# Kernel tuning notes

Measured on AMD Instinct MI355X. Metric: run time of the kernel, lower is better.

## Reference

```python
import jax, jax.numpy as jnp
import numpy as np

N = 50000      # nodes
DEG = 32       # fixed out-degree used to build a synthetic CSR graph
E = N * DEG    # edges
F = 64         # in_feats = n_hidden = out_feats
K = 3          # n_kernels
DIM = 2        # pseudo-coordinate projection dim
L = 3          # n_layers + 1 GMMConv layers


def setup_inputs() -> dict:
    key = jax.random.key(0)
    ks = jax.random.split(key, 8)
    feat = jax.random.normal(ks[0], (N, F), jnp.float32)
    pseudo = jax.random.uniform(ks[1], (E, 2), jnp.float32)  # per-edge pseudo coords
    rowptr = jnp.arange(N + 1, dtype=jnp.int32) * DEG        # CSR row pointers
    colind = jax.random.randint(ks[2], (E,), 0, N, jnp.int32)  # neighbor (src) ids
    # Per-layer parameters, stacked over L layers (all layers are FxF here).
    proj_W = 0.5 * jax.random.normal(ks[3], (L, 2, DIM), jnp.float32)   # pseudo_proj Linear weight
    proj_b = jnp.zeros((L, DIM), jnp.float32)                            # pseudo_proj Linear bias
    fc_W = jax.random.normal(ks[4], (L, F, K * F), jnp.float32) / np.sqrt(F)  # GMMConv fc (no bias)
    mu = jax.random.normal(ks[5], (L, K, DIM), jnp.float32)              # Gaussian means
    inv_sigma = jnp.ones((L, K, DIM), jnp.float32)                       # inverse std-devs
    return {"feat": feat, "pseudo": pseudo, "rowptr": rowptr, "colind": colind,
            "proj_W": proj_W, "proj_b": proj_b, "fc_W": fc_W, "mu": mu,
            "inv_sigma": inv_sigma}


def reference(feat, pseudo, rowptr, colind, proj_W, proj_b, fc_W, mu, inv_sigma):
    n = feat.shape[0]
    e = colind.shape[0]
    n_layers = fc_W.shape[0]
    n_kern = mu.shape[1]
    # dst node of each edge from CSR rowptr (edge e belongs to row i iff rowptr[i] <= e < rowptr[i+1])
    dst = jnp.searchsorted(rowptr, jnp.arange(e, dtype=rowptr.dtype), side="right") - 1

    h = feat
    for i in range(n_layers):  # small fixed layer loop
        # pseudo_proj: Linear(2, dim) + Tanh, per edge -> [E, DIM]
        u = jnp.tanh(pseudo @ proj_W[i] + proj_b[i])
        # Gaussian kernel weights: w[e,k] = exp(-0.5 * sum_d ((u - mu)^2 * inv_sigma^2)) -> [E, K]
        diff = u[:, None, :] - mu[i][None, :, :]
        w = jnp.exp(-0.5 * jnp.sum(diff * diff * (inv_sigma[i][None, :, :] ** 2), axis=-1))
        out_dim = fc_W[i].shape[1] // n_kern
        hp = (h @ fc_W[i]).reshape(n, n_kern, out_dim)  # [N, K, out]
        # message per edge: sum_k w[e,k] * hp[src(e), k, :]; loop over small K to avoid [E,K,out]
        msg = jnp.zeros((e, out_dim), h.dtype)
        for k in range(n_kern):
            msg = msg + w[:, k:k + 1] * hp[colind, k, :]
        # scatter-reduce (sum aggregation) into destination nodes
        h = jax.ops.segment_sum(msg, dst, num_segments=n)
        # dropout is identity in eval mode (p=0.0)
    return h
```

## Files before the change

kernel.cpp:

```cpp
#include <hip/hip_runtime.h>
#include <math.h>

#define FEAT 64
#define NKERN 3

typedef __attribute__((ext_vector_type(8))) short short8;
typedef __attribute__((ext_vector_type(4))) float float4v;
typedef __attribute__((ext_vector_type(2))) float float2v;

__device__ __forceinline__ unsigned short f2bf(float f) {
    unsigned int u = __float_as_uint(f);
    u = (u + 0x7fffu + ((u >> 16) & 1u)) >> 16;
    return (unsigned short)u;
}
__device__ __forceinline__ float bf2f(unsigned short b) {
    return __uint_as_float(((unsigned int)b) << 16);
}
__device__ __forceinline__ float fast_tanh(float x) {
    float e = __expf(2.f * x);
    return fmaf(-2.f, __builtin_amdgcn_rcpf(e + 1.f), 1.f);
}
__device__ __forceinline__ float sxor16(float v) {
    return __shfl_xor(v, 16, 64);
}

__global__ __launch_bounds__(256) void prep_kernel(
    const float* __restrict__ x, unsigned short* __restrict__ y, int n4,
    const float* __restrict__ fcW,
    unsigned short* __restrict__ Bth, unsigned short* __restrict__ Btl,
    int totalW, int nCastBlocks)
{
    int b = blockIdx.x;
    if (b < nCastBlocks) {
        int i = b * 256 + threadIdx.x;
        if (i >= n4) return;
        float4 v = ((const float4*)x)[i];
        ushort4 o;
        o.x = f2bf(v.x); o.y = f2bf(v.y); o.z = f2bf(v.z); o.w = f2bf(v.w);
        ((ushort4*)y)[i] = o;
    } else {
        int idx = (b - nCastBlocks) * 256 + threadIdx.x;
        if (idx >= totalW) return;
        int l   = idx / (FEAT * 192);
        int rem = idx - l * (FEAT * 192);
        int f   = rem / 192;
        int jp  = rem - f * 192;
        int k = jp >> 6, j = jp & 63;
        float v = fcW[(size_t)l * 12288 + j * 192 + k * 64 + f];
        unsigned short hi = f2bf(v);
        int dst = l * 12288 +
                  ((((f >> 4) * 6 + (jp >> 5)) * 4 + ((jp >> 3) & 3)) * 16 + (f & 15)) * 8 +
                  (jp & 7);
        Bth[dst] = hi;
        Btl[dst] = f2bf(v - bf2f(hi));
    }
}

__global__ __launch_bounds__(512, 8) void layer_kernel(
    const unsigned short* __restrict__ h,
    const int*   __restrict__ rowptr,
    const int*   __restrict__ colind,
    const float* __restrict__ pseudo,
    const float* __restrict__ projW,
    const float* __restrict__ projB,
    const float* __restrict__ mu,
    const float* __restrict__ isg,
    int layer,
    const unsigned short* __restrict__ Bth,
    const unsigned short* __restrict__ Btl,
    float* __restrict__ out,
    unsigned short* __restrict__ hnext,
    int n_nodes, int last_layer)
{
    __shared__ __align__(16) unsigned short Atile[3264];
    __shared__ __align__(16) unsigned int   Wlds[8][2][132];
    int tid  = threadIdx.x;
    int wv   = tid >> 6;
    int lane = tid & 63;
    int t0   = blockIdx.x * 16;

    const float* pw = projW + layer * 4;
    const float* pb = projB + layer * 2;
    const float* mm = mu  + layer * 6;
    const float* ss = isg + layer * 6;
    float pw0 = pw[0], pw1 = pw[1], pw2 = pw[2], pw3 = pw[3];
    float pb0 = pb[0], pb1 = pb[1];
    float m0 = mm[0], m1 = mm[1], m2 = mm[2], m3 = mm[3], m4 = mm[4], m5 = mm[5];
    float c0 = -0.5f * ss[0] * ss[0], c1 = -0.5f * ss[1] * ss[1];
    float c2 = -0.5f * ss[2] * ss[2], c3 = -0.5f * ss[3] * ss[3];
    float c4 = -0.5f * ss[4] * ss[4], c5 = -0.5f * ss[5] * ss[5];

    int half = lane >> 5;
    int p    = lane & 31;
    const char* hb = (const char*)h;

    int node = t0 + wv * 2 + half;
    int ncl  = node < n_nodes - 1 ? node : (n_nodes - 1);
    int rp   = rowptr[ncl];
    int deg  = rowptr[ncl + 1] - rp;
    bool fast = __all((deg == 32) && (node < n_nodes));
    if (fast) {
        int ei = rp + p;
        int cc = colind[ei];
        float2 ps = ((const float2*)pseudo)[ei];
        float u0 = fast_tanh(fmaf(ps.x, pw0, fmaf(ps.y, pw2, pb0)));
        float u1 = fast_tanh(fmaf(ps.x, pw1, fmaf(ps.y, pw3, pb1)));
        float d0 = u0 - m0, d1 = u1 - m1;
        float w0v = __expf(fmaf(d0 * d0, c0, d1 * d1 * c1));
        d0 = u0 - m2; d1 = u1 - m3;
        float w1v = __expf(fmaf(d0 * d0, c2, d1 * d1 * c3));
        d0 = u0 - m4; d1 = u1 - m5;
        float w2v = __expf(fmaf(d0 * d0, c4, d1 * d1 * c5));
        uint4 recw;
        recw.x = ((unsigned int)cc) << 7;
        recw.y = __float_as_uint(w0v);
        recw.z = __float_as_uint(w1v);
        recw.w = __float_as_uint(w2v);
        *(uint4*)&Wlds[wv][half][p * 4] = recw;

        int sub = (lane >> 4) & 1;
        int ch  = lane & 15;
        unsigned int fo = (unsigned int)(ch * 8);
        const unsigned int* Wg = &Wlds[wv][half][0];

        float2v a0l = {0.f,0.f}, a0h = {0.f,0.f};
        float2v a1l = {0.f,0.f}, a1h = {0.f,0.f};
        float2v a2l = {0.f,0.f}, a2h = {0.f,0.f};

        #pragma unroll
        for (int i = 0; i < 16; ++i) {
            int e = sub * 16 + i;
            uint4 rc = *(const uint4*)(Wg + e * 4);
            uint2 hv = *(const uint2*)(hb + (rc.x + fo));
            float2v vlo, vhi;
            vlo.x = __uint_as_float(hv.x << 16);
            vlo.y = __uint_as_float(hv.x & 0xffff0000u);
            vhi.x = __uint_as_float(hv.y << 16);
            vhi.y = __uint_as_float(hv.y & 0xffff0000u);
            float w0 = __uint_as_float(rc.y);
            float w1 = __uint_as_float(rc.z);
            float w2 = __uint_as_float(rc.w);
            float2v s0 = {w0, w0}, s1 = {w1, w1}, s2 = {w2, w2};
            a0l = __builtin_elementwise_fma(vlo, s0, a0l);
            a0h = __builtin_elementwise_fma(vhi, s0, a0h);
            a1l = __builtin_elementwise_fma(vlo, s1, a1l);
            a1h = __builtin_elementwise_fma(vhi, s1, a1h);
            a2l = __builtin_elementwise_fma(vlo, s2, a2l);
            a2h = __builtin_elementwise_fma(vhi, s2, a2h);
        }

        a0l.x += sxor16(a0l.x); a0l.y += sxor16(a0l.y);
        a0h.x += sxor16(a0h.x); a0h.y += sxor16(a0h.y);
        a1l.x += sxor16(a1l.x); a1l.y += sxor16(a1l.y);
        a1h.x += sxor16(a1h.x); a1h.y += sxor16(a1h.y);
        a2l.x += sxor16(a2l.x); a2l.y += sxor16(a2l.y);
        a2h.x += sxor16(a2h.x); a2h.y += sxor16(a2h.y);

        if (sub == 0) {
            int m  = wv * 2 + half;
            int j0 = ch * 4;
            int sa = (j0 >> 5) * 544 + ((j0 >> 3) & 3) * 136 + m * 8 + (j0 & 7);
            unsigned int k0l, k0h, k1l, k1h, k2l, k2h;
            asm("v_cvt_pk_bf16_f32 %0, %1, %2" : "=v"(k0l) : "v"(a0l.x), "v"(a0l.y));
            asm("v_cvt_pk_bf16_f32 %0, %1, %2" : "=v"(k0h) : "v"(a0h.x), "v"(a0h.y));
            asm("v_cvt_pk_bf16_f32 %0, %1, %2" : "=v"(k1l) : "v"(a1l.x), "v"(a1l.y));
            asm("v_cvt_pk_bf16_f32 %0, %1, %2" : "=v"(k1h) : "v"(a1h.x), "v"(a1h.y));
            asm("v_cvt_pk_bf16_f32 %0, %1, %2" : "=v"(k2l) : "v"(a2l.x), "v"(a2l.y));
            asm("v_cvt_pk_bf16_f32 %0, %1, %2" : "=v"(k2h) : "v"(a2h.x), "v"(a2h.y));
            uint2 w0 = {k0l, k0h}, w1 = {k1l, k1h}, w2 = {k2l, k2h};
            *(uint2*)&Atile[sa]        = w0;
            *(uint2*)&Atile[sa + 1088] = w1;
            *(uint2*)&Atile[sa + 2176] = w2;
        }
    } else {
        for (int mq = 0; mq < 2; ++mq) {
            int node2 = t0 + wv * 2 + mq;
            float a0 = 0.f, a1 = 0.f, a2 = 0.f;
            if (node2 < n_nodes) {
                int nu = __builtin_amdgcn_readfirstlane(node2);
                int r0 = rowptr[nu];
                int dg = rowptr[nu + 1] - r0;
                for (int i = 0; i < dg; ++i) {
                    int cc = colind[r0 + i];
                    float px = pseudo[(size_t)(r0 + i) * 2];
                    float py = pseudo[(size_t)(r0 + i) * 2 + 1];
                    float u0 = fast_tanh(fmaf(px, pw0, fmaf(py, pw2, pb0)));
                    float u1 = fast_tanh(fmaf(px, pw1, fmaf(py, pw3, pb1)));
                    float d0 = u0 - m0, d1 = u1 - m1;
                    float w0e = __expf(fmaf(d0 * d0, c0, d1 * d1 * c1));
                    d0 = u0 - m2; d1 = u1 - m3;
                    float w1e = __expf(fmaf(d0 * d0, c2, d1 * d1 * c3));
                    d0 = u0 - m4; d1 = u1 - m5;
                    float w2e = __expf(fmaf(d0 * d0, c4, d1 * d1 * c5));
                    float vf = bf2f(h[(size_t)cc * FEAT + lane]);
                    a0 = fmaf(w0e, vf, a0);
                    a1 = fmaf(w1e, vf, a1);
                    a2 = fmaf(w2e, vf, a2);
                }
            }
            int sb = (lane >> 5) * 544 + ((lane >> 3) & 3) * 136 + (wv * 2 + mq) * 8 + (lane & 7);
            Atile[sb]        = f2bf(a0);
            Atile[sb + 1088] = f2bf(a1);
            Atile[sb + 2176] = f2bf(a2);
        }
    }
    __syncthreads();

    if (wv < 4) {
        int q  = lane >> 4;
        int nn = lane & 15;
        const unsigned short* bt0 = Bth + (((wv * 6) * 4 + q) * 16 + nn) * 8;
        const unsigned short* bt1 = Btl + (((wv * 6) * 4 + q) * 16 + nn) * 8;
        float4v acc = (float4v){0.f, 0.f, 0.f, 0.f};
        #pragma unroll
        for (int ks = 0; ks < 6; ++ks) {
            short8 ah = *(const short8*)&Atile[ks * 544 + q * 136 + nn * 8];
            short8 bh = *(const short8*)(bt0 + ks * 512);
            short8 bl = *(const short8*)(bt1 + ks * 512);
            acc = __builtin_amdgcn_mfma_f32_16x16x32_bf16(ah, bh, acc, 0, 0, 0);
            acc = __builtin_amdgcn_mfma_f32_16x16x32_bf16(ah, bl, acc, 0, 0, 0);
        }
        #pragma unroll
        for (int r = 0; r < 4; ++r) {
            int row = t0 + q * 4 + r;
            if (row < n_nodes) {
                if (last_layer)
                    out[(size_t)row * 64 + wv * 16 + nn] = acc[r];
                else
                    hnext[(size_t)row * 64 + wv * 16 + nn] = f2bf(acc[r]);
            }
        }
    }
}

extern "C" void kernel_launch(void* const* d_in, const int* in_sizes, int n_in,
                              void* d_out, int out_size, void* d_ws, size_t ws_size,
                              hipStream_t stream)
{
    const float* feat   = (const float*)d_in[0];
    const float* pseudo = (const float*)d_in[1];
    const int*   rowptr = (const int*)d_in[2];
    const int*   colind = (const int*)d_in[3];
    const float* projW  = (const float*)d_in[4];
    const float* projB  = (const float*)d_in[5];
    const float* fcW    = (const float*)d_in[6];
    const float* mu     = (const float*)d_in[7];
    const float* isg    = (const float*)d_in[8];
    float* out = (float*)d_out;

    int n  = in_sizes[0] / FEAT;
    int n_layers = in_sizes[6] / (FEAT * NKERN * FEAT);

    unsigned short* hbA = (unsigned short*)d_ws;
    unsigned short* hbB = hbA + (size_t)n * FEAT;
    unsigned short* Bth = hbB + (size_t)n * FEAT;
    unsigned short* Btl = Bth + (size_t)n_layers * 12288;

    int n4 = n * FEAT / 4;
    int totalW = n_layers * FEAT * 192;
    int castBlocks = (n4 + 255) / 256;
    int wpBlocks   = (totalW + 255) / 256;

    dim3 blk(256);
    dim3 prepGrid(castBlocks + wpBlocks);
    dim3 layerGrid((n + 15) / 16);
    dim3 layerBlk(512);

    prep_kernel<<<prepGrid, blk, 0, stream>>>(
        feat, hbA, n4, fcW, Bth, Btl, totalW, castBlocks);

    const unsigned short* hin = hbA;
    for (int l = 0; l < n_layers; ++l) {
        int last = (l == n_layers - 1);
        unsigned short* hb_out = (l == 0) ? hbB : hbA;
        layer_kernel<<<layerGrid, layerBlk, 0, stream>>>(
            hin, rowptr, colind, pseudo, projW, projB, mu, isg, l,
            Bth + (size_t)l * 12288, Btl + (size_t)l * 12288,
            out, hb_out, n, last);
        hin = hb_out;
    }
}
```

Before: 172.2 us.

## Split fused gather+MFMA layer kernel into separate gather and matmul kernels

```diff
diff --git a/kernel.cpp b/kernel.cpp
--- a/kernel.cpp
+++ b/kernel.cpp
@@ -56,7 +56,7 @@
     }
 }
 
-__global__ __launch_bounds__(512, 8) void layer_kernel(
+__global__ __launch_bounds__(512, 8) void gather_kernel(
     const unsigned short* __restrict__ h,
     const int*   __restrict__ rowptr,
     const int*   __restrict__ colind,
@@ -66,18 +66,15 @@
     const float* __restrict__ mu,
     const float* __restrict__ isg,
     int layer,
-    const unsigned short* __restrict__ Bth,
-    const unsigned short* __restrict__ Btl,
-    float* __restrict__ out,
-    unsigned short* __restrict__ hnext,
-    int n_nodes, int last_layer)
-{
-    __shared__ __align__(16) unsigned short Atile[3264];
-    __shared__ __align__(16) unsigned int   Wlds[8][2][132];
+    unsigned short* __restrict__ agg,
+    int n_nodes)
+{
+    __shared__ __align__(16) unsigned int Wlds[8][2][132];
     int tid  = threadIdx.x;
     int wv   = tid >> 6;
     int lane = tid & 63;
     int t0   = blockIdx.x * 16;
+    unsigned short* at = agg + (size_t)blockIdx.x * 3072;
 
     const float* pw = projW + layer * 4;
     const float* pb = projB + layer * 2;
@@ -159,7 +156,7 @@
         if (sub == 0) {
             int m  = wv * 2 + half;
             int j0 = ch * 4;
-            int sa = (j0 >> 5) * 544 + ((j0 >> 3) & 3) * 136 + m * 8 + (j0 & 7);
+            int sa = (j0 >> 5) * 512 + ((j0 >> 3) & 3) * 128 + m * 8 + (j0 & 7);
             unsigned int k0l, k0h, k1l, k1h, k2l, k2h;
             asm("v_cvt_pk_bf16_f32 %0, %1, %2" : "=v"(k0l) : "v"(a0l.x), "v"(a0l.y));
             asm("v_cvt_pk_bf16_f32 %0, %1, %2" : "=v"(k0h) : "v"(a0h.x), "v"(a0h.y));
@@ -168,9 +165,9 @@
             asm("v_cvt_pk_bf16_f32 %0, %1, %2" : "=v"(k2l) : "v"(a2l.x), "v"(a2l.y));
             asm("v_cvt_pk_bf16_f32 %0, %1, %2" : "=v"(k2h) : "v"(a2h.x), "v"(a2h.y));
             uint2 w0 = {k0l, k0h}, w1 = {k1l, k1h}, w2 = {k2l, k2h};
-            *(uint2*)&Atile[sa]        = w0;
-            *(uint2*)&Atile[sa + 1088] = w1;
-            *(uint2*)&Atile[sa + 2176] = w2;
+            *(uint2*)&at[sa]        = w0;
+            *(uint2*)&at[sa + 1024] = w1;
+            *(uint2*)&at[sa + 2048] = w2;
         }
     } else {
         for (int mq = 0; mq < 2; ++mq) {
@@ -198,37 +195,49 @@
                     a2 = fmaf(w2e, vf, a2);
                 }
             }
-            int sb = (lane >> 5) * 544 + ((lane >> 3) & 3) * 136 + (wv * 2 + mq) * 8 + (lane & 7);
-            Atile[sb]        = f2bf(a0);
-            Atile[sb + 1088] = f2bf(a1);
-            Atile[sb + 2176] = f2bf(a2);
-        }
-    }
-    __syncthreads();
-
-    if (wv < 4) {
-        int q  = lane >> 4;
-        int nn = lane & 15;
-        const unsigned short* bt0 = Bth + (((wv * 6) * 4 + q) * 16 + nn) * 8;
-        const unsigned short* bt1 = Btl + (((wv * 6) * 4 + q) * 16 + nn) * 8;
-        float4v acc = (float4v){0.f, 0.f, 0.f, 0.f};
-        #pragma unroll
-        for (int ks = 0; ks < 6; ++ks) {
-            short8 ah = *(const short8*)&Atile[ks * 544 + q * 136 + nn * 8];
-            short8 bh = *(const short8*)(bt0 + ks * 512);
-            short8 bl = *(const short8*)(bt1 + ks * 512);
-            acc = __builtin_amdgcn_mfma_f32_16x16x32_bf16(ah, bh, acc, 0, 0, 0);
-            acc = __builtin_amdgcn_mfma_f32_16x16x32_bf16(ah, bl, acc, 0, 0, 0);
-        }
-        #pragma unroll
-        for (int r = 0; r < 4; ++r) {
-            int row = t0 + q * 4 + r;
-            if (row < n_nodes) {
-                if (last_layer)
-                    out[(size_t)row * 64 + wv * 16 + nn] = acc[r];
-                else
-                    hnext[(size_t)row * 64 + wv * 16 + nn] = f2bf(acc[r]);
-            }
+            int mm2 = wv * 2 + mq;
+            int sb = (lane >> 5) * 512 + ((lane >> 3) & 3) * 128 + mm2 * 8 + (lane & 7);
+            at[sb]        = f2bf(a0);
+            at[sb + 1024] = f2bf(a1);
+            at[sb + 2048] = f2bf(a2);
+        }
+    }
+}
+
+__global__ __launch_bounds__(256) void mm_kernel(
+    const unsigned short* __restrict__ agg,
+    const unsigned short* __restrict__ Bth,
+    const unsigned short* __restrict__ Btl,
+    float* __restrict__ out,
+    unsigned short* __restrict__ hnext,
+    int n_nodes, int last_layer)
+{
+    int wv   = threadIdx.x >> 6;
+    int lane = threadIdx.x & 63;
+    int t0   = blockIdx.x * 16;
+    const unsigned short* at = agg + (size_t)blockIdx.x * 3072;
+
+    int q  = lane >> 4;
+    int nn = lane & 15;
+    const unsigned short* bt0 = Bth + (((wv * 6) * 4 + q) * 16 + nn) * 8;
+    const unsigned short* bt1 = Btl + (((wv * 6) * 4 + q) * 16 + nn) * 8;
+    float4v acc = (float4v){0.f, 0.f, 0.f, 0.f};
+    #pragma unroll
+    for (int ks = 0; ks < 6; ++ks) {
+        short8 ah = *(const short8*)&at[ks * 512 + q * 128 + nn * 8];
+        short8 bh = *(const short8*)(bt0 + ks * 512);
+        short8 bl = *(const short8*)(bt1 + ks * 512);
+        acc = __builtin_amdgcn_mfma_f32_16x16x32_bf16(ah, bh, acc, 0, 0, 0);
+        acc = __builtin_amdgcn_mfma_f32_16x16x32_bf16(ah, bl, acc, 0, 0, 0);
+    }
+    #pragma unroll
+    for (int r = 0; r < 4; ++r) {
+        int row = t0 + q * 4 + r;
+        if (row < n_nodes) {
+            if (last_layer)
+                out[(size_t)row * 64 + wv * 16 + nn] = acc[r];
+            else
+                hnext[(size_t)row * 64 + wv * 16 + nn] = f2bf(acc[r]);
         }
     }
 }
@@ -250,11 +259,13 @@
 
     int n  = in_sizes[0] / FEAT;
     int n_layers = in_sizes[6] / (FEAT * NKERN * FEAT);
+    int ntiles = (n + 15) / 16;
 
     unsigned short* hbA = (unsigned short*)d_ws;
     unsigned short* hbB = hbA + (size_t)n * FEAT;
     unsigned short* Bth = hbB + (size_t)n * FEAT;
     unsigned short* Btl = Bth + (size_t)n_layers * 12288;
+    unsigned short* agg = Btl + (size_t)n_layers * 12288;
 
     int n4 = n * FEAT / 4;
     int totalW = n_layers * FEAT * 192;
@@ -263,8 +274,6 @@
 
     dim3 blk(256);
     dim3 prepGrid(castBlocks + wpBlocks);
-    dim3 layerGrid((n + 15) / 16);
-    dim3 layerBlk(512);
 
     prep_kernel<<<prepGrid, blk, 0, stream>>>(
         feat, hbA, n4, fcW, Bth, Btl, totalW, castBlocks);
@@ -273,9 +282,10 @@
     for (int l = 0; l < n_layers; ++l) {
         int last = (l == n_layers - 1);
         unsigned short* hb_out = (l == 0) ? hbB : hbA;
-        layer_kernel<<<layerGrid, layerBlk, 0, stream>>>(
-            hin, rowptr, colind, pseudo, projW, projB, mu, isg, l,
-            Bth + (size_t)l * 12288, Btl + (size_t)l * 12288,
+        gather_kernel<<<dim3(ntiles), dim3(512), 0, stream>>>(
+            hin, rowptr, colind, pseudo, projW, projB, mu, isg, l, agg, n);
+        mm_kernel<<<dim3(ntiles), dim3(256), 0, stream>>>(
+            agg, Bth + (size_t)l * 12288, Btl + (size_t)l * 12288,
             out, hb_out, n, last);
         hin = hb_out;
     }
```

After: 192.2 us. 1.12x slower.
